# Optimization experiments

Measured on AMD Instinct MI355X. Metric: run time of the kernel, lower is better.

## Reference

```python
import jax, jax.numpy as jnp
import numpy as np

B, XL, QL, VL, D = 8, 128, 16, 256, 256


def setup_inputs() -> dict:
    key = jax.random.key(0)
    ks = jax.random.split(key, 10)
    q = jax.random.normal(ks[0], (B, XL, QL, D), dtype=jnp.float32)
    k = jax.random.normal(ks[1], (B, XL, VL, D), dtype=jnp.float32)
    v = jax.random.normal(ks[2], (B, XL, VL, D), dtype=jnp.float32)
    # mask==True means position is masked out (filled with -10 before softmax)
    mask = jax.random.bernoulli(ks[3], 0.3, (B, XL, VL))
    s = 1.0 / np.sqrt(D)
    qw_w = jax.random.uniform(ks[4], (D, D), jnp.float32, -s, s)
    qw_b = jax.random.uniform(ks[5], (D,), jnp.float32, -s, s)
    kw_w = jax.random.uniform(ks[6], (D, D), jnp.float32, -s, s)
    kw_b = jax.random.uniform(ks[7], (D,), jnp.float32, -s, s)
    vw_w = jax.random.uniform(ks[8], (D, D), jnp.float32, -s, s)
    vw_b = jax.random.uniform(ks[9], (D,), jnp.float32, -s, s)
    return {"q": q, "k": k, "v": v, "mask": mask,
            "qw_w": qw_w, "qw_b": qw_b, "kw_w": kw_w, "kw_b": kw_b,
            "vw_w": vw_w, "vw_b": vw_b}


def reference(q, k, v, mask, qw_w, qw_b, kw_w, kw_b, vw_w, vw_b):
    # Linear projections (torch Linear: x @ W.T + b)
    qp = q @ qw_w.T + qw_b          # [b, x_l, q_l, d]
    kp = k @ kw_w.T + kw_b          # [b, x_l, v_l, d]
    vp = v @ vw_w.T + vw_b          # [b, x_l, v_l, d]
    # QK^T then max-pool over the q_l axis -> one score per value token
    scores = jnp.einsum('bxqd,bxvd->bxqv', qp, kp)   # [b, x_l, q_l, v_l]
    ta = jnp.max(scores, axis=-2)                    # [b, x_l, v_l]
    # L2-normalize over v_l (computed BEFORE masking, as in the original)
    ta = ta / jnp.linalg.norm(ta, axis=-1, keepdims=True)
    # rows where every position is masked (no words)
    nowords = jnp.sum(~mask, axis=-1) == 0           # [b, x_l]
    ta = jnp.where(mask, jnp.float32(-10.0), ta)
    attn = jax.nn.softmax(ta, axis=-1)               # [b, x_l, v_l]
    attn = jnp.where(nowords[..., None], jnp.float32(0.0), attn)
    out = jnp.einsum('bxv,bxvd->bxd', attn, vp)      # [b, x_l, d]
    return out[:, :, None, :]                        # [b, x_l, 1, d]
```

## Files before the change

### kernel.cpp

```cpp
#include <hip/hip_runtime.h>
#include <hip/hip_bf16.h>

#define NPAIR 1024
#define DD    256
#define QL    16
#define VL    256
#define KSTR  264

#define WS_MB   1024
#define WS_U    2048
#define WS_MT   4096
#define WS_TA   135168

typedef __bf16 bf16x8 __attribute__((ext_vector_type(8)));
typedef __bf16 bf16x4 __attribute__((ext_vector_type(4)));
typedef float  f32x4  __attribute__((ext_vector_type(4)));

__global__ __launch_bounds__(256) void sa_precompute(const float* __restrict__ qw,
                                                     const float* __restrict__ qb,
                                                     const float* __restrict__ kw,
                                                     const float* __restrict__ kb,
                                                     const unsigned int* __restrict__ maskw,
                                                     char* __restrict__ ws) {
    int c = blockIdx.x, e = threadIdx.x;
    float acc = 0.f;
    #pragma unroll 16
    for (int d = 0; d < 256; ++d) acc += qw[d*256 + e] * kw[d*256 + c];
    ((__bf16*)(ws + WS_MT))[c*256 + e] = (__bf16)acc;
    if (c == 0) {
        float a2 = 0.f;
        #pragma unroll 16
        for (int d = 0; d < 256; ++d) a2 += qb[d] * kw[d*256 + e];
        ((float*)(ws + WS_MB))[e] = a2;
    } else if (c == 1) {
        float a2 = 0.f;
        #pragma unroll 16
        for (int d = 0; d < 256; ++d) a2 += qw[d*256 + e] * kb[d];
        ((float*)(ws + WS_U))[e] = a2;
    } else if (c == 2 && e == 0) {
        float a2 = 0.f;
        #pragma unroll 16
        for (int d = 0; d < 256; ++d) a2 += qb[d] * kb[d];
        ((float*)(ws + 4))[0] = a2;
    } else if (c == 3) {
        __shared__ int f;
        if (e == 0) f = 0;
        __syncthreads();
        if (maskw[e] & ~1u) atomicOr(&f, 1);
        __syncthreads();
        if (e == 0) *(int*)ws = f;
    }
}

__device__ __forceinline__ float blockReduceSum(float v, float* red, int tid) {
    __syncthreads();
    #pragma unroll
    for (int off = 32; off >= 1; off >>= 1) v += __shfl_xor(v, off);
    if ((tid & 63) == 0) red[tid >> 6] = v;
    __syncthreads();
    return (red[0] + red[1]) + (red[2] + red[3]);
}

__global__ __launch_bounds__(256) void sa_qk_ta(const float* __restrict__ qg,
                                                const float* __restrict__ kg,
                                                const char*  __restrict__ ws,
                                                float* __restrict__ ta_ws) {
    const int bid  = blockIdx.x;
    const int p    = bid >> 1;
    const int h    = bid & 1;
    const int tid  = threadIdx.x;
    const int lane = tid & 63;
    const int w    = tid >> 6;
    const int col  = lane & 15;
    const int quad = lane >> 4;

    const float  s0  = *(const float*)(ws + 4);
    const float* mb  = (const float*)(ws + WS_MB);
    const float* u   = (const float*)(ws + WS_U);
    const __bf16* MT = (const __bf16*)(ws + WS_MT);

    const float* Q = qg + (size_t)p * (QL * DD);
    const float* K = kg + (size_t)p * (VL * DD);

    __shared__ __align__(16) __bf16 q_lds[16 * KSTR];
    __shared__ __align__(16) __bf16 qk_lds[16 * KSTR];
    __shared__ __align__(16) float part[256];
    __shared__ float sbias_lds[16];

    {
        const float4* Q4 = (const float4*)Q;
        #pragma unroll
        for (int it = 0; it < 4; ++it) {
            int idx = tid + it * 256;
            float4 v4 = Q4[idx];
            int f = idx * 4; int i = f >> 8; int e = f & 255;
            bf16x4 t; t[0] = (__bf16)v4.x; t[1] = (__bf16)v4.y;
                      t[2] = (__bf16)v4.z; t[3] = (__bf16)v4.w;
            *(bf16x4*)(&q_lds[i * KSTR + e]) = t;
        }
    }
    {
        int i = tid >> 4, seg = tid & 15;
        float s = 0.f;
        const float* qrow = Q + i * DD + seg * 16;
        const float* useg = u + seg * 16;
        #pragma unroll
        for (int e = 0; e < 16; ++e) s += qrow[e] * useg[e];
        part[i * 16 + seg] = s;
    }
    __syncthreads();
    if (tid < 16) {
        float s = s0;
        #pragma unroll
        for (int seg = 0; seg < 16; ++seg) s += part[tid * 16 + seg];
        sbias_lds[tid] = s;
    }

    {
        #pragma unroll
        for (int t = 0; t < 4; ++t) {
            int cc = (w * 4 + t) * 16 + col;
            float mbv = mb[cc];
            f32x4 acc; acc[0] = mbv; acc[1] = mbv; acc[2] = mbv; acc[3] = mbv;
            const __bf16* arow = &q_lds[col * KSTR + quad * 8];
            const __bf16* brow = &MT[(size_t)cc * 256 + quad * 8];
            #pragma unroll
            for (int k0 = 0; k0 < 256; k0 += 32) {
                bf16x8 a = *(const bf16x8*)(arow + k0);
                bf16x8 b = *(const bf16x8*)(brow + k0);
                acc = __builtin_amdgcn_mfma_f32_16x16x32_bf16(a, b, acc, 0, 0, 0);
            }
            #pragma unroll
            for (int r = 0; r < 4; ++r)
                qk_lds[(quad * 4 + r) * KSTR + cc] = (__bf16)acc[r];
        }
    }
    __syncthreads();

    {
        bf16x8 afrag[8];
        #pragma unroll
        for (int s = 0; s < 8; ++s)
            afrag[s] = *(const bf16x8*)(&qk_lds[col * KSTR + quad * 8 + s * 32]);

        #pragma unroll 1
        for (int vt = 0; vt < 2; ++vt) {
            int vrow = h * 128 + vt * 64 + w * 16 + col;
            const float* Krow = K + (size_t)vrow * DD + quad * 8;
            float4 b0[8], b1[8];
            #pragma unroll
            for (int s = 0; s < 8; ++s) {
                b0[s] = *(const float4*)(Krow + s * 32);
                b1[s] = *(const float4*)(Krow + s * 32 + 4);
            }
            f32x4 acc;
            #pragma unroll
            for (int r = 0; r < 4; ++r) acc[r] = sbias_lds[quad * 4 + r];
            #pragma unroll
            for (int s = 0; s < 8; ++s) {
                bf16x8 b;
                b[0] = (__bf16)b0[s].x; b[1] = (__bf16)b0[s].y;
                b[2] = (__bf16)b0[s].z; b[3] = (__bf16)b0[s].w;
                b[4] = (__bf16)b1[s].x; b[5] = (__bf16)b1[s].y;
                b[6] = (__bf16)b1[s].z; b[7] = (__bf16)b1[s].w;
                acc = __builtin_amdgcn_mfma_f32_16x16x32_bf16(afrag[s], b, acc, 0, 0, 0);
            }
            float m4 = fmaxf(fmaxf(acc[0], acc[1]), fmaxf(acc[2], acc[3]));
            m4 = fmaxf(m4, __shfl_xor(m4, 16));
            m4 = fmaxf(m4, __shfl_xor(m4, 32));
            if (quad == 0) ta_ws[(size_t)p * 256 + vrow] = m4;
        }
    }
}

__global__ __launch_bounds__(256) void sa_out(const float* __restrict__ vg,
                                              const void*  __restrict__ maskp,
                                              const float* __restrict__ vww,
                                              const float* __restrict__ vwb,
                                              const char*  __restrict__ ws,
                                              const float* __restrict__ ta_ws,
                                              float* __restrict__ outp) {
    const int p   = blockIdx.x;
    const int tid = threadIdx.x;
    const int flag = *(const int*)ws;

    const float* V = vg + (size_t)p * (VL * DD);

    __shared__ __align__(16) float attn_lds[256];
    __shared__ __align__(16) float w_lds[256];
    __shared__ float red[4];

    float myv = ta_ws[(size_t)p * 256 + tid];
    float ssq = blockReduceSum(myv * myv, red, tid);
    float rn  = 1.0f / sqrtf(ssq);
    bool masked;
    if (flag) masked = ((const unsigned char*)maskp)[(size_t)p * 256 + tid] != 0;
    else      masked = ((const int*)maskp)[(size_t)p * 256 + tid] != 0;
    float cnt = blockReduceSum(masked ? 0.f : 1.f, red, tid);
    float val = masked ? -10.f : (myv * rn);
    float ex  = expf(val);
    float se  = blockReduceSum(ex, red, tid);
    float S    = (cnt == 0.f) ? 0.f : 1.f;
    float attn = (cnt == 0.f) ? 0.f : (ex / se);
    attn_lds[tid] = attn;
    __syncthreads();

    {
        float acc = 0.f;
        #pragma unroll 1
        for (int ch = 0; ch < 8; ++ch) {
            float r[32];
            const float* Vb = V + (size_t)(ch * 32) * DD + tid;
            #pragma unroll
            for (int j = 0; j < 32; ++j) r[j] = Vb[(size_t)j * DD];
            #pragma unroll
            for (int j = 0; j < 32; ++j) acc += attn_lds[ch * 32 + j] * r[j];
        }
        w_lds[tid] = acc;
    }
    __syncthreads();

    {
        float accO = vwb[tid] * S;
        const float* row = vww + (size_t)tid * 256;
        #pragma unroll 8
        for (int c = 0; c < 256; c += 4) {
            float4 wv = *(const float4*)&w_lds[c];
            float4 m4 = *(const float4*)&row[c];
            accO += wv.x * m4.x + wv.y * m4.y + wv.z * m4.z + wv.w * m4.w;
        }
        outp[(size_t)p * 256 + tid] = accO;
    }
}

extern "C" void kernel_launch(void* const* d_in, const int* in_sizes, int n_in,
                              void* d_out, int out_size, void* d_ws, size_t ws_size,
                              hipStream_t stream) {
    const float* q    = (const float*)d_in[0];
    const float* k    = (const float*)d_in[1];
    const float* v    = (const float*)d_in[2];
    const void*  mask = d_in[3];
    const float* qw_w = (const float*)d_in[4];
    const float* qw_b = (const float*)d_in[5];
    const float* kw_w = (const float*)d_in[6];
    const float* kw_b = (const float*)d_in[7];
    const float* vw_w = (const float*)d_in[8];
    const float* vw_b = (const float*)d_in[9];

    char*  ws    = (char*)d_ws;
    float* ta_ws = (float*)(ws + WS_TA);

    hipLaunchKernelGGL(sa_precompute, dim3(256), dim3(256), 0, stream,
                       qw_w, qw_b, kw_w, kw_b, (const unsigned int*)mask, ws);
    hipLaunchKernelGGL(sa_qk_ta, dim3(2 * NPAIR), dim3(256), 0, stream,
                       q, k, (const char*)ws, ta_ws);
    hipLaunchKernelGGL(sa_out, dim3(NPAIR), dim3(256), 0, stream,
                       v, mask, vw_w, vw_b, (const char*)ws, (const float*)ta_ws,
                       (float*)d_out);
}
```

Baseline: 578.0 us.

## Fuse QK max-pool and attention output kernels into one per-pair kernel

Result: faster. 555.0 us (-4.0%).

```diff
diff --git a/kernel.cpp b/kernel.cpp
--- a/kernel.cpp
+++ b/kernel.cpp
@@ -10,7 +10,7 @@
 #define WS_MB   1024
 #define WS_U    2048
 #define WS_MT   4096
-#define WS_TA   135168
+#define WS_VWT  135168
 
 typedef __bf16 bf16x8 __attribute__((ext_vector_type(8)));
 typedef __bf16 bf16x4 __attribute__((ext_vector_type(4)));
@@ -20,6 +20,7 @@
                                                      const float* __restrict__ qb,
                                                      const float* __restrict__ kw,
                                                      const float* __restrict__ kb,
+                                                     const float* __restrict__ vww,
                                                      const unsigned int* __restrict__ maskw,
                                                      char* __restrict__ ws) {
     int c = blockIdx.x, e = threadIdx.x;
@@ -27,6 +28,9 @@
     #pragma unroll 16
     for (int d = 0; d < 256; ++d) acc += qw[d*256 + e] * kw[d*256 + c];
     ((__bf16*)(ws + WS_MT))[c*256 + e] = (__bf16)acc;
+
+    ((float*)(ws + WS_VWT))[(c >> 2)*1024 + e*4 + (c & 3)] = vww[e*256 + c];
+
     if (c == 0) {
         float a2 = 0.f;
         #pragma unroll 16
@@ -61,31 +65,39 @@
     return (red[0] + red[1]) + (red[2] + red[3]);
 }
 
-__global__ __launch_bounds__(256) void sa_qk_ta(const float* __restrict__ qg,
+__global__ __launch_bounds__(256) void sa_fused(const float* __restrict__ qg,
                                                 const float* __restrict__ kg,
+                                                const float* __restrict__ vg,
+                                                const void*  __restrict__ maskp,
+                                                const float* __restrict__ vwb,
                                                 const char*  __restrict__ ws,
-                                                float* __restrict__ ta_ws) {
-    const int bid  = blockIdx.x;
-    const int p    = bid >> 1;
-    const int h    = bid & 1;
+                                                float* __restrict__ outp) {
+    const int p    = blockIdx.x;
     const int tid  = threadIdx.x;
     const int lane = tid & 63;
     const int w    = tid >> 6;
     const int col  = lane & 15;
     const int quad = lane >> 4;
 
-    const float  s0  = *(const float*)(ws + 4);
-    const float* mb  = (const float*)(ws + WS_MB);
-    const float* u   = (const float*)(ws + WS_U);
-    const __bf16* MT = (const __bf16*)(ws + WS_MT);
+    const int    flag = *(const int*)ws;
+    const float  s0   = *(const float*)(ws + 4);
+    const float* mb   = (const float*)(ws + WS_MB);
+    const float* u    = (const float*)(ws + WS_U);
+    const __bf16* MT  = (const __bf16*)(ws + WS_MT);
 
     const float* Q = qg + (size_t)p * (QL * DD);
     const float* K = kg + (size_t)p * (VL * DD);
+    const float* V = vg + (size_t)p * (VL * DD);
 
     __shared__ __align__(16) __bf16 q_lds[16 * KSTR];
     __shared__ __align__(16) __bf16 qk_lds[16 * KSTR];
     __shared__ __align__(16) float part[256];
     __shared__ float sbias_lds[16];
+    __shared__ __align__(16) float ta_lds[256];
+    __shared__ __align__(16) float attn_lds[256];
+    __shared__ __align__(16) float wpart[4][256];
+    __shared__ __align__(16) float w_lds[256];
+    __shared__ float red[4];
 
     {
         const float4* Q4 = (const float4*)Q;
@@ -144,8 +156,8 @@
             afrag[s] = *(const bf16x8*)(&qk_lds[col * KSTR + quad * 8 + s * 32]);
 
         #pragma unroll 1
-        for (int vt = 0; vt < 2; ++vt) {
-            int vrow = h * 128 + vt * 64 + w * 16 + col;
+        for (int vt = 0; vt < 4; ++vt) {
+            int vrow = vt * 64 + w * 16 + col;
             const float* Krow = K + (size_t)vrow * DD + quad * 8;
             float4 b0[8], b1[8];
             #pragma unroll
@@ -168,67 +180,54 @@
             float m4 = fmaxf(fmaxf(acc[0], acc[1]), fmaxf(acc[2], acc[3]));
             m4 = fmaxf(m4, __shfl_xor(m4, 16));
             m4 = fmaxf(m4, __shfl_xor(m4, 32));
-            if (quad == 0) ta_ws[(size_t)p * 256 + vrow] = m4;
-        }
-    }
-}
-
-__global__ __launch_bounds__(256) void sa_out(const float* __restrict__ vg,
-                                              const void*  __restrict__ maskp,
-                                              const float* __restrict__ vww,
-                                              const float* __restrict__ vwb,
-                                              const char*  __restrict__ ws,
-                                              const float* __restrict__ ta_ws,
-                                              float* __restrict__ outp) {
-    const int p   = blockIdx.x;
-    const int tid = threadIdx.x;
-    const int flag = *(const int*)ws;
-
-    const float* V = vg + (size_t)p * (VL * DD);
-
-    __shared__ __align__(16) float attn_lds[256];
-    __shared__ __align__(16) float w_lds[256];
-    __shared__ float red[4];
-
-    float myv = ta_ws[(size_t)p * 256 + tid];
-    float ssq = blockReduceSum(myv * myv, red, tid);
-    float rn  = 1.0f / sqrtf(ssq);
-    bool masked;
-    if (flag) masked = ((const unsigned char*)maskp)[(size_t)p * 256 + tid] != 0;
-    else      masked = ((const int*)maskp)[(size_t)p * 256 + tid] != 0;
-    float cnt = blockReduceSum(masked ? 0.f : 1.f, red, tid);
-    float val = masked ? -10.f : (myv * rn);
-    float ex  = expf(val);
-    float se  = blockReduceSum(ex, red, tid);
-    float S    = (cnt == 0.f) ? 0.f : 1.f;
-    float attn = (cnt == 0.f) ? 0.f : (ex / se);
-    attn_lds[tid] = attn;
-    __syncthreads();
-
-    {
-        float acc = 0.f;
-        #pragma unroll 1
-        for (int ch = 0; ch < 8; ++ch) {
-            float r[32];
-            const float* Vb = V + (size_t)(ch * 32) * DD + tid;
-            #pragma unroll
-            for (int j = 0; j < 32; ++j) r[j] = Vb[(size_t)j * DD];
-            #pragma unroll
-            for (int j = 0; j < 32; ++j) acc += attn_lds[ch * 32 + j] * r[j];
-        }
-        w_lds[tid] = acc;
-    }
-    __syncthreads();
-
-    {
-        float accO = vwb[tid] * S;
-        const float* row = vww + (size_t)tid * 256;
+            if (quad == 0) ta_lds[vrow] = m4;
+        }
+    }
+    __syncthreads();
+
+    float S;
+    {
+        float myv = ta_lds[tid];
+        float ssq = blockReduceSum(myv * myv, red, tid);
+        float rn  = 1.0f / sqrtf(ssq);
+        bool masked;
+        if (flag) masked = ((const unsigned char*)maskp)[(size_t)p * 256 + tid] != 0;
+        else      masked = ((const int*)maskp)[(size_t)p * 256 + tid] != 0;
+        float cnt = blockReduceSum(masked ? 0.f : 1.f, red, tid);
+        float val = masked ? -10.f : (myv * rn);
+        float ex  = expf(val);
+        float se  = blockReduceSum(ex, red, tid);
+        S = (cnt == 0.f) ? 0.f : 1.f;
+        attn_lds[tid] = (cnt == 0.f) ? 0.f : (ex / se);
+    }
+    __syncthreads();
+
+    {
+        const f32x4* V4 = (const f32x4*)V;
+        f32x4 wa; wa[0] = 0.f; wa[1] = 0.f; wa[2] = 0.f; wa[3] = 0.f;
+        #pragma unroll 4
+        for (int j = 0; j < 64; ++j) {
+            int row = (j << 2) | w;
+            float a = attn_lds[row];
+            f32x4 r4 = V4[row * 64 + lane];
+            wa += a * r4;
+        }
+        *(f32x4*)&wpart[w][lane * 4] = wa;
+    }
+    __syncthreads();
+    w_lds[tid] = (wpart[0][tid] + wpart[1][tid]) + (wpart[2][tid] + wpart[3][tid]);
+    __syncthreads();
+
+    {
+        const f32x4* T4 = (const f32x4*)(ws + WS_VWT);
+        f32x4 acc4; acc4[0] = 0.f; acc4[1] = 0.f; acc4[2] = 0.f; acc4[3] = 0.f;
         #pragma unroll 8
-        for (int c = 0; c < 256; c += 4) {
-            float4 wv = *(const float4*)&w_lds[c];
-            float4 m4 = *(const float4*)&row[c];
-            accO += wv.x * m4.x + wv.y * m4.y + wv.z * m4.z + wv.w * m4.w;
-        }
+        for (int cq = 0; cq < 64; ++cq) {
+            f32x4 m4 = T4[cq * 256 + tid];
+            f32x4 wv = *(const f32x4*)&w_lds[cq * 4];
+            acc4 += m4 * wv;
+        }
+        float accO = vwb[tid] * S + (acc4[0] + acc4[1]) + (acc4[2] + acc4[3]);
         outp[(size_t)p * 256 + tid] = accO;
     }
 }
@@ -247,14 +246,10 @@
     const float* vw_w = (const float*)d_in[8];
     const float* vw_b = (const float*)d_in[9];
 
-    char*  ws    = (char*)d_ws;
-    float* ta_ws = (float*)(ws + WS_TA);
+    char* ws = (char*)d_ws;
 
     hipLaunchKernelGGL(sa_precompute, dim3(256), dim3(256), 0, stream,
-                       qw_w, qw_b, kw_w, kw_b, (const unsigned int*)mask, ws);
-    hipLaunchKernelGGL(sa_qk_ta, dim3(2 * NPAIR), dim3(256), 0, stream,
-                       q, k, (const char*)ws, ta_ws);
-    hipLaunchKernelGGL(sa_out, dim3(NPAIR), dim3(256), 0, stream,
-                       v, mask, vw_w, vw_b, (const char*)ws, (const float*)ta_ws,
-                       (float*)d_out);
-}
+                       qw_w, qw_b, kw_w, kw_b, vw_w, (const unsigned int*)mask, ws);
+    hipLaunchKernelGGL(sa_fused, dim3(NPAIR), dim3(256), 0, stream,
+                       q, k, v, mask, vw_b, (const char*)ws, (float*)d_out);
+}
```
